# Optimization experiments

Hardware: AMD Instinct MI355X
Metric: run time of the kernel (lower is better)

## Reference

```python
import jax, jax.numpy as jnp
import numpy as np

B, N, K, D = 4, 16384, 16, 16
EPS = 1e-6

def setup_inputs() -> dict:
    key = jax.random.key(0)
    ks = jax.random.split(key, 8)
    coords = jax.random.normal(ks[0], (B, N, 3), dtype=jnp.float32)
    features = jax.random.normal(ks[1], (B, D, N, 1), dtype=jnp.float32)
    idx = jax.random.randint(ks[2], (B, N, K), 0, N, dtype=jnp.int32)
    dist = jax.random.uniform(ks[3], (B, N, K), dtype=jnp.float32)
    conv_w = jax.random.normal(ks[4], (D, 10), dtype=jnp.float32) * 0.1  # 1x1 conv weight
    conv_b = jax.random.normal(ks[5], (D,), dtype=jnp.float32) * 0.1
    bn_gamma = jnp.ones((D,), dtype=jnp.float32)
    bn_beta = jnp.zeros((D,), dtype=jnp.float32)
    return {"coords": coords, "features": features, "idx": idx, "dist": dist,
            "conv_w": conv_w, "conv_b": conv_b, "bn_gamma": bn_gamma, "bn_beta": bn_beta}

def reference(coords, features, idx, dist, conv_w, conv_b, bn_gamma, bn_beta):
    # gather neighbor coords: (B, N, K, 3)
    neighbors = jax.vmap(lambda c, i: c[i])(coords, idx)
    center = jnp.broadcast_to(coords[:, :, None, :], (B, N, K, 3))
    # concat along channel: center(3) + neighbor(3) + relative(3) + dist(1) -> (B, N, K, 10)
    concat = jnp.concatenate([center, neighbors, center - neighbors, dist[..., None]], axis=-1)
    # 1x1 conv: (B, N, K, 10) x (D, 10) -> (B, D, N, K)
    x = jnp.einsum('bnkc,dc->bdnk', concat, conv_w) + conv_b[None, :, None, None]
    # BatchNorm2d (training-mode batch stats), eps=1e-6, per channel over (B, N, K)
    mean = jnp.mean(x, axis=(0, 2, 3), keepdims=True)
    var = jnp.mean(jnp.square(x - mean), axis=(0, 2, 3), keepdims=True)
    x = (x - mean) * jax.lax.rsqrt(var + EPS)
    x = x * bn_gamma[None, :, None, None] + bn_beta[None, :, None, None]
    x = jax.nn.relu(x)
    # concat with broadcast features -> (B, 2D, N, K)
    feats = jnp.broadcast_to(features, (B, D, N, K))
    return jnp.concatenate([x, feats], axis=1)
```

## Files before the change

kernel.cpp:

```cpp
#include <hip/hip_runtime.h>

#define BB 4
#define NN 16384
#define KK 16
#define DD 16
#define MTOT (BB*NN*KK)


__global__ __launch_bounds__(256) void lse_stats(
    const float* __restrict__ coords,
    const int*   __restrict__ idx,
    const float* __restrict__ dist,
    const float* __restrict__ conv_w,
    float* __restrict__ ws)
{
    __shared__ __align__(16) float wl[DD*8];
    __shared__ float red[4][32];
    const int tid = threadIdx.x;
    if (tid < DD*8) {
        int d = tid >> 3, c = tid & 7;
        float v = 0.f;
        if (c < 3)      v = conv_w[d*10+c] + conv_w[d*10+6+c];
        else if (c < 6) v = conv_w[d*10+c] - conv_w[d*10+c+3];
        else if (c == 6) v = conv_w[d*10+9];
        wl[tid] = v;
    }
    __syncthreads();

    const int g = blockIdx.x * 256 + tid;
    const int n = g & (NN - 1);
    const int b = g >> 14;

    const size_t cbase = (size_t)(b*NN + n) * 3;
    const float cx = coords[cbase+0], cy = coords[cbase+1], cz = coords[cbase+2];

    float ux[KK], uy[KK], uz[KK], ud[KK];
    const int4*   ip = (const int4*)  (idx  + (size_t)(b*NN + n) * KK);
    const float4* dp = (const float4*)(dist + (size_t)(b*NN + n) * KK);
    #pragma unroll
    for (int q = 0; q < 4; ++q) {
        int4  iv = ip[q];
        float4 dv = dp[q];
        int   js[4]  = {iv.x, iv.y, iv.z, iv.w};
        float dsv[4] = {dv.x, dv.y, dv.z, dv.w};
        #pragma unroll
        for (int t = 0; t < 4; ++t) {
            int k = q*4 + t;
            size_t nb = (size_t)(b*NN + js[t]) * 3;
            ux[k] = coords[nb+0];
            uy[k] = coords[nb+1];
            uz[k] = coords[nb+2];
            ud[k] = dsv[t];
        }
    }

    float sum[DD], ssq[DD];
    #pragma unroll
    for (int d = 0; d < DD; ++d) {
        float4 w0 = *(const float4*)&wl[d*8];
        float4 w1 = *(const float4*)&wl[d*8+4];
        float base = w0.x*cx + w0.y*cy + w0.z*cz;
        float s = 0.f, s2 = 0.f;
        #pragma unroll
        for (int k = 0; k < KK; ++k) {
            float dot = base + w0.w*ux[k] + w1.x*uy[k] + w1.y*uz[k] + w1.z*ud[k];
            s  += dot;
            s2  = fmaf(dot, dot, s2);
        }
        sum[d] = s; ssq[d] = s2;
    }

    #pragma unroll
    for (int d = 0; d < DD; ++d) {
        float s = sum[d], s2 = ssq[d];
        for (int off = 32; off > 0; off >>= 1) {
            s  += __shfl_down(s,  off);
            s2 += __shfl_down(s2, off);
        }
        sum[d] = s; ssq[d] = s2;
    }
    const int lane = tid & 63, wave = tid >> 6;
    if (lane == 0) {
        #pragma unroll
        for (int d = 0; d < DD; ++d) { red[wave][d] = sum[d]; red[wave][16+d] = ssq[d]; }
    }
    __syncthreads();
    if (tid < 32) {
        float v = red[0][tid] + red[1][tid] + red[2][tid] + red[3][tid];
        atomicAdd(&ws[tid], v);
    }
}

__global__ void lse_finalize(
    const float* __restrict__ conv_w,
    const float* __restrict__ gamma,
    const float* __restrict__ beta,
    float* __restrict__ ws)
{
    __shared__ float sc_s[DD], b2_s[DD];
    const int tid = threadIdx.x;
    if (tid < DD) {
        const float inv_m = 1.0f / (float)MTOT;
        float mean = ws[tid] * inv_m;
        float var  = ws[16+tid] * inv_m - mean*mean;
        float inv  = rsqrtf(var + 1e-6f);
        float sc   = gamma[tid] * inv;
        sc_s[tid] = sc;
        b2_s[tid] = beta[tid] - mean * sc;
    }
    __syncthreads();
    {
        int d = tid >> 3, c = tid & 7;
        float v = 0.f;
        if (c < 3)       v = conv_w[d*10+c] + conv_w[d*10+6+c];
        else if (c < 6)  v = conv_w[d*10+c] - conv_w[d*10+c+3];
        else if (c == 6) v = conv_w[d*10+9];
        ws[32 + tid] = (c == 7) ? b2_s[d] : v * sc_s[d];
    }
}

__global__ __launch_bounds__(256) void lse_write(
    const float* __restrict__ coords,
    const float* __restrict__ features,
    const int*   __restrict__ idx,
    const float* __restrict__ dist,
    const float* __restrict__ ws,
    float* __restrict__ out)
{
    __shared__ __align__(16) float wl[DD*8];
    const int tid = threadIdx.x;
    if (tid < DD*8) wl[tid] = ws[32 + tid];
    __syncthreads();

    const int g   = blockIdx.x * 256 + tid;
    const int kq  = g & 3;
    const int pos = g >> 2;
    const int n   = pos & (NN - 1);
    const int b   = pos >> 14;

    const size_t cbase = (size_t)(b*NN + n) * 3;
    const float cx = coords[cbase+0], cy = coords[cbase+1], cz = coords[cbase+2];

    const int4   iv = *(const int4*)  (idx  + ((size_t)(b*NN + n) * KK + kq*4));
    const float4 dv = *(const float4*)(dist + ((size_t)(b*NN + n) * KK + kq*4));

    float ux[4], uy[4], uz[4], ud[4];
    {
        int   js[4]  = {iv.x, iv.y, iv.z, iv.w};
        float dsv[4] = {dv.x, dv.y, dv.z, dv.w};
        #pragma unroll
        for (int t = 0; t < 4; ++t) {
            size_t nb = (size_t)(b*NN + js[t]) * 3;
            ux[t] = coords[nb+0];
            uy[t] = coords[nb+1];
            uz[t] = coords[nb+2];
            ud[t] = dsv[t];
        }
    }

    float* op = out + ((size_t)(b*2*DD) * NN + n) * KK + kq*4;

    #pragma unroll
    for (int d = 0; d < DD; ++d) {
        float4 w0 = *(const float4*)&wl[d*8];
        float4 w1 = *(const float4*)&wl[d*8+4];
        float base = w1.w + w0.x*cx + w0.y*cy + w0.z*cz;
        float4 v;
        v.x = fmaxf(base + w0.w*ux[0] + w1.x*uy[0] + w1.y*uz[0] + w1.z*ud[0], 0.f);
        v.y = fmaxf(base + w0.w*ux[1] + w1.x*uy[1] + w1.y*uz[1] + w1.z*ud[1], 0.f);
        v.z = fmaxf(base + w0.w*ux[2] + w1.x*uy[2] + w1.y*uz[2] + w1.z*ud[2], 0.f);
        v.w = fmaxf(base + w0.w*ux[3] + w1.x*uy[3] + w1.y*uz[3] + w1.z*ud[3], 0.f);
        *(float4*)(op + (size_t)d * NN * KK) = v;
    }

    #pragma unroll
    for (int d = 0; d < DD; ++d) {
        float f = features[(size_t)(b*DD + d) * NN + n];
        float4 v = {f, f, f, f};
        *(float4*)(op + (size_t)(DD + d) * NN * KK) = v;
    }
}

extern "C" void kernel_launch(void* const* d_in, const int* in_sizes, int n_in,
                              void* d_out, int out_size, void* d_ws, size_t ws_size,
                              hipStream_t stream)
{
    const float* coords   = (const float*)d_in[0];
    const float* features = (const float*)d_in[1];
    const int*   idx      = (const int*)  d_in[2];
    const float* dist     = (const float*)d_in[3];
    const float* conv_w   = (const float*)d_in[4];
    const float* gamma    = (const float*)d_in[6];
    const float* beta     = (const float*)d_in[7];
    float* ws  = (float*)d_ws;
    float* out = (float*)d_out;

    hipMemsetAsync(d_ws, 0, 32 * sizeof(float), stream);
    lse_stats   <<<BB*NN/256,        256, 0, stream>>>(coords, idx, dist, conv_w, ws);
    lse_finalize<<<1,                128, 0, stream>>>(conv_w, gamma, beta, ws);
    lse_write   <<<BB*NN*KK/4/256,   256, 0, stream>>>(coords, features, idx, dist, ws, out);
}
```

Measured before the change: 50.03 us.

## Compute BN stats via input Gram matrix with per-block partials and nontemporal stores

The stats kernel no longer evaluates all 16 conv channels per neighbor. It accumulates the 7-dim input moments (first moments plus a 28-entry second-moment Gram matrix) with 4 threads per point, and writes per-block partial sums instead of using atomics. The finalize kernel reduces the 1024 partials and turns the Gram matrix into per-channel mean and variance through the conv weights. This also removes the memset. Output writes in the write kernel use nontemporal stores to avoid cache pollution. The algebraic variance (E[x²]−mean²) over the Gram matrix may lose some float precision.

```diff
diff --git a/kernel.cpp b/kernel.cpp
--- a/kernel.cpp
+++ b/kernel.cpp
@@ -5,117 +5,171 @@
 #define KK 16
 #define DD 16
 #define MTOT (BB*NN*KK)
+#define NBLK_STATS 1024
+#define PACK_OFF (35*NBLK_STATS)
+
+typedef float f32x4 __attribute__((ext_vector_type(4)));
 
 
 __global__ __launch_bounds__(256) void lse_stats(
     const float* __restrict__ coords,
     const int*   __restrict__ idx,
     const float* __restrict__ dist,
-    const float* __restrict__ conv_w,
     float* __restrict__ ws)
 {
-    __shared__ __align__(16) float wl[DD*8];
-    __shared__ float red[4][32];
+    __shared__ float red[4][36];
     const int tid = threadIdx.x;
-    if (tid < DD*8) {
-        int d = tid >> 3, c = tid & 7;
-        float v = 0.f;
-        if (c < 3)      v = conv_w[d*10+c] + conv_w[d*10+6+c];
-        else if (c < 6) v = conv_w[d*10+c] - conv_w[d*10+c+3];
-        else if (c == 6) v = conv_w[d*10+9];
-        wl[tid] = v;
-    }
-    __syncthreads();
-
-    const int g = blockIdx.x * 256 + tid;
-    const int n = g & (NN - 1);
-    const int b = g >> 14;
-
-    const size_t cbase = (size_t)(b*NN + n) * 3;
-    const float cx = coords[cbase+0], cy = coords[cbase+1], cz = coords[cbase+2];
-
-    float ux[KK], uy[KK], uz[KK], ud[KK];
-    const int4*   ip = (const int4*)  (idx  + (size_t)(b*NN + n) * KK);
-    const float4* dp = (const float4*)(dist + (size_t)(b*NN + n) * KK);
-    #pragma unroll
-    for (int q = 0; q < 4; ++q) {
-        int4  iv = ip[q];
-        float4 dv = dp[q];
+    const int g   = blockIdx.x * 256 + tid;
+    const int kq  = g & 3;
+    const int pos = g >> 2;
+    const int n   = pos & (NN - 1);
+    const int b   = pos >> 14;
+
+    const size_t cb = (size_t)(b*NN + n) * 3;
+    const float c0 = coords[cb], c1 = coords[cb+1], c2 = coords[cb+2];
+
+    const int4   iv = *(const int4*)  (idx  + ((size_t)(b*NN + n) * KK + kq*4));
+    const float4 dv = *(const float4*)(dist + ((size_t)(b*NN + n) * KK + kq*4));
+
+    float u[4][4];
+    {
         int   js[4]  = {iv.x, iv.y, iv.z, iv.w};
-        float dsv[4] = {dv.x, dv.y, dv.z, dv.w};
+        float ds4[4] = {dv.x, dv.y, dv.z, dv.w};
         #pragma unroll
         for (int t = 0; t < 4; ++t) {
-            int k = q*4 + t;
             size_t nb = (size_t)(b*NN + js[t]) * 3;
-            ux[k] = coords[nb+0];
-            uy[k] = coords[nb+1];
-            uz[k] = coords[nb+2];
-            ud[k] = dsv[t];
-        }
-    }
-
-    float sum[DD], ssq[DD];
-    #pragma unroll
-    for (int d = 0; d < DD; ++d) {
-        float4 w0 = *(const float4*)&wl[d*8];
-        float4 w1 = *(const float4*)&wl[d*8+4];
-        float base = w0.x*cx + w0.y*cy + w0.z*cz;
-        float s = 0.f, s2 = 0.f;
-        #pragma unroll
-        for (int k = 0; k < KK; ++k) {
-            float dot = base + w0.w*ux[k] + w1.x*uy[k] + w1.y*uz[k] + w1.z*ud[k];
-            s  += dot;
-            s2  = fmaf(dot, dot, s2);
-        }
-        sum[d] = s; ssq[d] = s2;
-    }
-
-    #pragma unroll
-    for (int d = 0; d < DD; ++d) {
-        float s = sum[d], s2 = ssq[d];
-        for (int off = 32; off > 0; off >>= 1) {
-            s  += __shfl_down(s,  off);
-            s2 += __shfl_down(s2, off);
-        }
-        sum[d] = s; ssq[d] = s2;
-    }
-    const int lane = tid & 63, wave = tid >> 6;
-    if (lane == 0) {
-        #pragma unroll
-        for (int d = 0; d < DD; ++d) { red[wave][d] = sum[d]; red[wave][16+d] = ssq[d]; }
-    }
-    __syncthreads();
-    if (tid < 32) {
-        float v = red[0][tid] + red[1][tid] + red[2][tid] + red[3][tid];
-        atomicAdd(&ws[tid], v);
-    }
-}
-
-__global__ void lse_finalize(
+            u[0][t] = coords[nb+0];
+            u[1][t] = coords[nb+1];
+            u[2][t] = coords[nb+2];
+            u[3][t] = ds4[t];
+        }
+    }
+    float su[4];
+    #pragma unroll
+    for (int i = 0; i < 4; ++i) su[i] = (u[i][0]+u[i][1]) + (u[i][2]+u[i][3]);
+
+    float p[35];
+    p[0] = 4.f*c0; p[1] = 4.f*c1; p[2] = 4.f*c2;
+    p[3] = su[0];  p[4] = su[1];  p[5] = su[2]; p[6] = su[3];
+    {
+        const float c[3] = {c0, c1, c2};
+        #pragma unroll
+        for (int i = 0; i < 7; ++i) {
+            #pragma unroll
+            for (int j = i; j < 7; ++j) {
+                const int e = 7 + 7*i - (i*(i-1))/2 + (j - i);
+                float v;
+                if (j < 3)       v = 4.f * c[i] * c[j];
+                else if (i < 3)  v = c[i] * su[j-3];
+                else {
+                    v = 0.f;
+                    #pragma unroll
+                    for (int k = 0; k < 4; ++k) v = fmaf(u[i-3][k], u[j-3][k], v);
+                }
+                p[e] = v;
+            }
+        }
+    }
+
+    #pragma unroll
+    for (int e = 0; e < 35; ++e) {
+        p[e] += __shfl_xor(p[e], 1);
+        p[e] += __shfl_xor(p[e], 2);
+    }
+    const int lane = tid & 63, wave = tid >> 6, r = lane & 3;
+    float q[9];
+    #pragma unroll
+    for (int i = 0; i < 9; ++i) {
+        float v = p[4*i];
+        if (4*i+1 < 35) v = (r == 1) ? p[4*i+1] : v;
+        if (4*i+2 < 35) v = (r == 2) ? p[4*i+2] : v;
+        if (4*i+3 < 35) v = (r == 3) ? p[4*i+3] : v;
+        q[i] = v;
+    }
+    #pragma unroll
+    for (int i = 0; i < 9; ++i) {
+        q[i] += __shfl_down(q[i], 4);
+        q[i] += __shfl_down(q[i], 8);
+        q[i] += __shfl_down(q[i], 16);
+        q[i] += __shfl_down(q[i], 32);
+    }
+    if (lane < 4) {
+        #pragma unroll
+        for (int i = 0; i < 9; ++i) {
+            int e = 4*i + lane;
+            if (e < 35) red[wave][e] = q[i];
+        }
+    }
+    __syncthreads();
+    if (tid < 35) {
+        float v = (red[0][tid] + red[1][tid]) + (red[2][tid] + red[3][tid]);
+        ws[(size_t)tid * NBLK_STATS + blockIdx.x] = v;
+    }
+}
+
+__global__ __launch_bounds__(256) void lse_finalize(
     const float* __restrict__ conv_w,
     const float* __restrict__ gamma,
     const float* __restrict__ beta,
     float* __restrict__ ws)
 {
+    __shared__ float wsum[4][35];
+    __shared__ float gram[35];
     __shared__ float sc_s[DD], b2_s[DD];
-    const int tid = threadIdx.x;
+    const int tid = threadIdx.x, lane = tid & 63, wave = tid >> 6;
+
+    #pragma unroll
+    for (int e = 0; e < 35; ++e) {
+        const float* pe = ws + (size_t)e * NBLK_STATS;
+        float a = (pe[tid] + pe[tid+256]) + (pe[tid+512] + pe[tid+768]);
+        a += __shfl_down(a, 1);
+        a += __shfl_down(a, 2);
+        a += __shfl_down(a, 4);
+        a += __shfl_down(a, 8);
+        a += __shfl_down(a, 16);
+        a += __shfl_down(a, 32);
+        if (lane == 0) wsum[wave][e] = a;
+    }
+    __syncthreads();
+    if (tid < 35) gram[tid] = (wsum[0][tid] + wsum[1][tid]) + (wsum[2][tid] + wsum[3][tid]);
+    __syncthreads();
+
     if (tid < DD) {
+        const int d = tid;
+        float a[7];
+        #pragma unroll
+        for (int c = 0; c < 3; ++c) {
+            a[c]   = conv_w[d*10+c]   + conv_w[d*10+6+c];
+            a[3+c] = conv_w[d*10+3+c] - conv_w[d*10+6+c];
+        }
+        a[6] = conv_w[d*10+9];
+        float mean_n = 0.f, msq_n = 0.f;
+        #pragma unroll
+        for (int i = 0; i < 7; ++i) mean_n = fmaf(a[i], gram[i], mean_n);
+        #pragma unroll
+        for (int i = 0; i < 7; ++i) {
+            #pragma unroll
+            for (int j = i; j < 7; ++j) {
+                const int e = 7 + 7*i - (i*(i-1))/2 + (j - i);
+                const float coef = (i == j) ? 1.f : 2.f;
+                msq_n = fmaf(coef * a[i] * a[j], gram[e], msq_n);
+            }
+        }
         const float inv_m = 1.0f / (float)MTOT;
-        float mean = ws[tid] * inv_m;
-        float var  = ws[16+tid] * inv_m - mean*mean;
-        float inv  = rsqrtf(var + 1e-6f);
-        float sc   = gamma[tid] * inv;
-        sc_s[tid] = sc;
-        b2_s[tid] = beta[tid] - mean * sc;
-    }
-    __syncthreads();
-    {
-        int d = tid >> 3, c = tid & 7;
+        const float mean = mean_n * inv_m;
+        const float var  = msq_n * inv_m - mean * mean;
+        const float sc   = gamma[d] * rsqrtf(var + 1e-6f);
+        sc_s[d] = sc;
+        b2_s[d] = beta[d] - mean * sc;
+    }
+    __syncthreads();
+    if (tid < 128) {
+        const int d = tid >> 3, cc = tid & 7;
         float v = 0.f;
-        if (c < 3)       v = conv_w[d*10+c] + conv_w[d*10+6+c];
-        else if (c < 6)  v = conv_w[d*10+c] - conv_w[d*10+c+3];
-        else if (c == 6) v = conv_w[d*10+9];
-        ws[32 + tid] = (c == 7) ? b2_s[d] : v * sc_s[d];
+        if (cc < 3)       v = conv_w[d*10+cc] + conv_w[d*10+6+cc];
+        else if (cc < 6)  v = conv_w[d*10+cc] - conv_w[d*10+cc+3];
+        else if (cc == 6) v = conv_w[d*10+9];
+        ws[PACK_OFF + tid] = (cc == 7) ? b2_s[d] : v * sc_s[d];
     }
 }
 
@@ -129,7 +183,7 @@
 {
     __shared__ __align__(16) float wl[DD*8];
     const int tid = threadIdx.x;
-    if (tid < DD*8) wl[tid] = ws[32 + tid];
+    if (tid < DD*8) wl[tid] = ws[PACK_OFF + tid];
     __syncthreads();
 
     const int g   = blockIdx.x * 256 + tid;
@@ -165,19 +219,19 @@
         float4 w0 = *(const float4*)&wl[d*8];
         float4 w1 = *(const float4*)&wl[d*8+4];
         float base = w1.w + w0.x*cx + w0.y*cy + w0.z*cz;
-        float4 v;
+        f32x4 v;
         v.x = fmaxf(base + w0.w*ux[0] + w1.x*uy[0] + w1.y*uz[0] + w1.z*ud[0], 0.f);
         v.y = fmaxf(base + w0.w*ux[1] + w1.x*uy[1] + w1.y*uz[1] + w1.z*ud[1], 0.f);
         v.z = fmaxf(base + w0.w*ux[2] + w1.x*uy[2] + w1.y*uz[2] + w1.z*ud[2], 0.f);
         v.w = fmaxf(base + w0.w*ux[3] + w1.x*uy[3] + w1.y*uz[3] + w1.z*ud[3], 0.f);
-        *(float4*)(op + (size_t)d * NN * KK) = v;
+        __builtin_nontemporal_store(v, (f32x4*)(op + (size_t)d * NN * KK));
     }
 
     #pragma unroll
     for (int d = 0; d < DD; ++d) {
         float f = features[(size_t)(b*DD + d) * NN + n];
-        float4 v = {f, f, f, f};
-        *(float4*)(op + (size_t)(DD + d) * NN * KK) = v;
+        f32x4 v = {f, f, f, f};
+        __builtin_nontemporal_store(v, (f32x4*)(op + (size_t)(DD + d) * NN * KK));
     }
 }
 
@@ -195,8 +249,7 @@
     float* ws  = (float*)d_ws;
     float* out = (float*)d_out;
 
-    hipMemsetAsync(d_ws, 0, 32 * sizeof(float), stream);
-    lse_stats   <<<BB*NN/256,        256, 0, stream>>>(coords, idx, dist, conv_w, ws);
-    lse_finalize<<<1,                128, 0, stream>>>(conv_w, gamma, beta, ws);
-    lse_write   <<<BB*NN*KK/4/256,   256, 0, stream>>>(coords, features, idx, dist, ws, out);
-}
+    lse_stats   <<<NBLK_STATS, 256, 0, stream>>>(coords, idx, dist, ws);
+    lse_finalize<<<1,          256, 0, stream>>>(conv_w, gamma, beta, ws);
+    lse_write   <<<BB*NN*KK/4/256, 256, 0, stream>>>(coords, features, idx, dist, ws, out);
+}
```

New measurement: 70.74 us. 1.41x slower.
